# Kernel tuning notes

Measured on AMD Instinct MI355X. Metric: run time of the kernel, lower is better.

Reference implementation:

```python
import jax, jax.numpy as jnp
import numpy as np


def setup_inputs() -> dict:
    key = jax.random.key(0)
    ks = jax.random.split(key, 7)
    G, MC, B = 4, 100, 512
    IN, H, OUT = 456, 400, 10
    return {
        "x": jax.random.normal(ks[0], (B, IN), dtype=jnp.float32),
        "mu1": jax.random.normal(ks[1], (G, IN, H), dtype=jnp.float32),
        "sigma1": jax.random.normal(ks[2], (G, IN, H), dtype=jnp.float32),
        "mu3": jax.random.normal(ks[3], (G, H, OUT), dtype=jnp.float32),
        "sigma3": jax.random.normal(ks[4], (G, H, OUT), dtype=jnp.float32),
        "zeta1": jax.random.normal(ks[5], (G, MC, B, H), dtype=jnp.float32),
        "zeta3": jax.random.normal(ks[6], (G, MC, B, OUT), dtype=jnp.float32),
        "num": 3,
    }


def reference(x, mu1, sigma1, mu3, sigma3, zeta1, zeta3, num):
    # softplus(sigma)^2, the local-reparameterization variance term
    sp2 = lambda s: jnp.square(jnp.log1p(jnp.exp(s)))

    def one_net(m1, s1, m3, s3, z1, z3):
        # layer 1: local reparameterization trick (Kingma et al. 2015)
        g1 = x @ m1                               # [B, H]
        d1 = (x * x) @ sp2(s1)                    # [B, H]
        h = jax.nn.relu(g1 + jnp.sqrt(d1) * z1)   # [MC, B, H] via broadcast
        # layer 2
        g3 = jnp.einsum('mbh,ho->mbo', h, m3)     # [MC, B, OUT]
        d3 = jnp.einsum('mbh,ho->mbo', h * h, sp2(s3))
        o = jax.nn.relu(g3 + jnp.sqrt(d3) * z3)
        p = jax.nn.softmax(o, axis=-1)            # nn.Softmax over class dim
        return p.mean(axis=0)                     # average over MC samples

    G = num + 1
    outs = jax.vmap(one_net)(mu1[:G], sigma1[:G], mu3[:G], sigma3[:G],
                             zeta1[:G], zeta3[:G])  # [G, B, OUT]
    B = x.shape[0]
    # torch.cat((out_0, out_1, ...), dim=1)
    return jnp.transpose(outs, (1, 0, 2)).reshape(B, -1)
```

## Files before the change

### kernel.cpp

```cpp
#include <hip/hip_runtime.h>
#include <math.h>

#define GN  4
#define MCN 100
#define BN  512
#define INN 456
#define HN  400
#define ON  10

__device__ __forceinline__ float sp2f(float s) {
    float l = log1pf(__expf(-fabsf(s)));
    float r = fmaxf(s, 0.0f) + l;
    return r * r;
}

#define DPP_ADD(v, CTRL) \
    ((v) + __int_as_float(__builtin_amdgcn_update_dpp( \
        0, __float_as_int(v), (CTRL), 0xF, 0xF, true)))

__device__ __forceinline__ float reduce16(float v) {
    v = DPP_ADD(v, 0xB1);
    v = DPP_ADD(v, 0x4E);
    v = DPP_ADD(v, 0x124);
    v = DPP_ADD(v, 0x128);
    return v;
}

__global__ __launch_bounds__(256) void k_transpose(
    const float* __restrict__ x, float* __restrict__ xT, float* __restrict__ xxT) {
    __shared__ float tile[64][65];
    int it = blockIdx.x;
    int bt = blockIdx.y;
    int tx = threadIdx.x & 63;
    int ty = threadIdx.x >> 6;
    int i_in = it * 64 + tx;
    #pragma unroll
    for (int r = 0; r < 16; ++r) {
        int row = r * 4 + ty;
        int b = bt * 64 + row;
        tile[row][tx] = (i_in < INN) ? x[b * INN + i_in] : 0.0f;
    }
    __syncthreads();
    #pragma unroll
    for (int r = 0; r < 16; ++r) {
        int row = r * 4 + ty;
        int i = it * 64 + row;
        if (i < INN) {
            float v = tile[tx][row];
            xT[i * BN + bt * 64 + tx]  = v;
            xxT[i * BN + bt * 64 + tx] = v * v;
        }
    }
}

__global__ __launch_bounds__(256) void k_sp(
    const float* __restrict__ sigma1, const float* __restrict__ sigma3,
    float* __restrict__ sp1, float* __restrict__ sp3) {
    int idx = blockIdx.x * 256 + threadIdx.x;
    const int n1 = GN * INN * HN / 4;
    const int n3 = GN * HN * ON / 4;
    if (idx < n1) {
        float4 s = ((const float4*)sigma1)[idx];
        float4 o;
        o.x = sp2f(s.x); o.y = sp2f(s.y); o.z = sp2f(s.z); o.w = sp2f(s.w);
        ((float4*)sp1)[idx] = o;
    } else if (idx < n1 + n3) {
        int k = idx - n1;
        float4 s = ((const float4*)sigma3)[k];
        float4 o;
        o.x = sp2f(s.x); o.y = sp2f(s.y); o.z = sp2f(s.z); o.w = sp2f(s.w);
        ((float4*)sp3)[k] = o;
    }
}

__global__ __launch_bounds__(256) void k_layer1(
    const float* __restrict__ xT, const float* __restrict__ xxT,
    const float* __restrict__ mu1, const float* __restrict__ sp1,
    float* __restrict__ A, float* __restrict__ S) {
    int bt = blockIdx.x;
    int ht = blockIdx.y;
    int g  = blockIdx.z;
    int lane = threadIdx.x & 63;
    int wv   = threadIdx.x >> 6;
    int h = ht * 64 + lane;
    bool hv = h < HN;
    int hc = hv ? h : (HN - 1);
    int b0 = __builtin_amdgcn_readfirstlane(bt * 16 + wv * 4);
    const float* mp = mu1 + (size_t)g * INN * HN + hc;
    const float* pp = sp1 + (size_t)g * INN * HN + hc;
    float accA[4] = {0.f, 0.f, 0.f, 0.f};
    float accD[4] = {0.f, 0.f, 0.f, 0.f};
    #pragma unroll 4
    for (int k = 0; k < INN; ++k) {
        float a = mp[(size_t)k * HN];
        float p = pp[(size_t)k * HN];
        float4 xv  = *(const float4*)(xT  + k * BN + b0);
        float4 xxv = *(const float4*)(xxT + k * BN + b0);
        accA[0] = fmaf(a, xv.x,  accA[0]);
        accA[1] = fmaf(a, xv.y,  accA[1]);
        accA[2] = fmaf(a, xv.z,  accA[2]);
        accA[3] = fmaf(a, xv.w,  accA[3]);
        accD[0] = fmaf(p, xxv.x, accD[0]);
        accD[1] = fmaf(p, xxv.y, accD[1]);
        accD[2] = fmaf(p, xxv.z, accD[2]);
        accD[3] = fmaf(p, xxv.w, accD[3]);
    }
    if (hv) {
        #pragma unroll
        for (int j = 0; j < 4; ++j) {
            size_t o = ((size_t)g * BN + (b0 + j)) * HN + h;
            A[o] = accA[j];
            S[o] = sqrtf(accD[j]);
        }
    }
}

template<int NI>
__device__ __forceinline__ void mc_chunk(
    int g, int b, int mb, int kc, int og, int rgg, int t,
    const float* __restrict__ zeta1, const float* __restrict__ zeta3,
    const float* as_s, const float* wp, float* epi, float* psum) {
    float acc[NI][ON];
    #pragma unroll
    for (int i = 0; i < NI; ++i)
        #pragma unroll
        for (int o = 0; o < ON; ++o) acc[i][o] = 0.0f;

    const float* zp[NI];
    #pragma unroll
    for (int i = 0; i < NI; ++i) {
        int m = mb + rgg + 8 * i;
        int mcl = m < MCN ? m : (MCN - 1);
        zp[i] = zeta1 + ((size_t)(g * MCN + mcl) * BN + b) * HN + kc;
    }

    float zc[NI];
    #pragma unroll
    for (int i = 0; i < NI; ++i) zc[i] = zp[i][0];

    #pragma unroll 1
    for (int j = 0; j < 25; ++j) {
        float zn[NI];
        if (j < 24) {
            #pragma unroll
            for (int i = 0; i < NI; ++i) zn[i] = zp[i][16 * (j + 1)];
        } else {
            #pragma unroll
            for (int i = 0; i < NI; ++i) zn[i] = 0.0f;
        }
        float2 as = *(const float2*)(as_s + 2 * (kc + 16 * j));
        const float* wr = wp + j * 160;
        float2 w01 = *(const float2*)(wr);
        float2 w23 = *(const float2*)(wr + 2);
        float2 w45 = *(const float2*)(wr + 4);
        float2 w67 = *(const float2*)(wr + 6);
        float2 w89 = *(const float2*)(wr + 8);
        #pragma unroll
        for (int i = 0; i < NI; ++i) {
            float hv = fmaxf(0.0f, fmaf(as.y, zc[i], as.x));
            float c = og ? hv * hv : hv;
            acc[i][0] = fmaf(c, w01.x, acc[i][0]);
            acc[i][1] = fmaf(c, w01.y, acc[i][1]);
            acc[i][2] = fmaf(c, w23.x, acc[i][2]);
            acc[i][3] = fmaf(c, w23.y, acc[i][3]);
            acc[i][4] = fmaf(c, w45.x, acc[i][4]);
            acc[i][5] = fmaf(c, w45.y, acc[i][5]);
            acc[i][6] = fmaf(c, w67.x, acc[i][6]);
            acc[i][7] = fmaf(c, w67.y, acc[i][7]);
            acc[i][8] = fmaf(c, w89.x, acc[i][8]);
            acc[i][9] = fmaf(c, w89.y, acc[i][9]);
        }
        #pragma unroll
        for (int i = 0; i < NI; ++i) zc[i] = zn[i];
    }

    #pragma unroll
    for (int i = 0; i < NI; ++i)
        #pragma unroll
        for (int o = 0; o < ON; ++o) acc[i][o] = reduce16(acc[i][o]);

    if (kc == 0) {
        #pragma unroll
        for (int i = 0; i < NI; ++i) {
            int rl = rgg + 8 * i;
            #pragma unroll
            for (int o = 0; o < ON; ++o)
                epi[(rl * ON + o) * 2 + og] = acc[i][o];
        }
    }
    __syncthreads();

    const int NR = NI * 8;
    if (t < NR) {
        int m = mb + t;
        if (m < MCN) {
            const float* z3p = zeta3 + ((size_t)(g * MCN + m) * BN + b) * ON;
            float ov[ON];
            float mx = 0.0f;
            #pragma unroll
            for (int o = 0; o < ON; ++o) {
                float2 gd = *(const float2*)(epi + (t * ON + o) * 2);
                float v = fmaf(sqrtf(gd.y), z3p[o], gd.x);
                v = fmaxf(v, 0.0f);
                ov[o] = v;
                mx = fmaxf(mx, v);
            }
            float se = 0.0f;
            #pragma unroll
            for (int o = 0; o < ON; ++o) { float e = __expf(ov[o] - mx); ov[o] = e; se += e; }
            float r = 1.0f / se;
            #pragma unroll
            for (int o = 0; o < ON; ++o) psum[o] = fmaf(ov[o], r, psum[o]);
        }
    }
    __syncthreads();
}

__global__ __launch_bounds__(256, 4) void k_layer2(
    const float* __restrict__ A, const float* __restrict__ S,
    const float* __restrict__ mu3, const float* __restrict__ sp3,
    const float* __restrict__ zeta1, const float* __restrict__ zeta3,
    float* __restrict__ out) {
    int b = blockIdx.x;
    int g = blockIdx.y;

    __shared__ __align__(16) float w_s[HN * ON];
    __shared__ __align__(16) float v_s[HN * ON];
    __shared__ __align__(16) float as_s[2 * HN];
    __shared__ __align__(16) float epi[32 * ON * 2];
    __shared__ __align__(16) float psh[32 * ON];

    int t = threadIdx.x;

    {
        const float4* wsrc = (const float4*)(mu3 + (size_t)g * HN * ON);
        const float4* vsrc = (const float4*)(sp3 + (size_t)g * HN * ON);
        for (int i = t; i < HN * ON / 4; i += 256) {
            ((float4*)w_s)[i] = wsrc[i];
            ((float4*)v_s)[i] = vsrc[i];
        }
    }
    for (int i = t; i < HN; i += 256) {
        size_t src = ((size_t)g * BN + b) * HN + i;
        as_s[2 * i]     = A[src];
        as_s[2 * i + 1] = S[src];
    }
    __syncthreads();

    int kc  = t & 15;
    int og  = (t >> 4) & 1;
    int rgg = t >> 5;

    const float* wp = (og ? v_s : w_s) + kc * ON;

    float psum[ON];
    #pragma unroll
    for (int o = 0; o < ON; ++o) psum[o] = 0.0f;

    #pragma unroll 1
    for (int c = 0; c < 3; ++c)
        mc_chunk<4>(g, b, c * 32, kc, og, rgg, t, zeta1, zeta3, as_s, wp, epi, psum);
    mc_chunk<1>(g, b, 96, kc, og, rgg, t, zeta1, zeta3, as_s, wp, epi, psum);

    if (t < 32) {
        #pragma unroll
        for (int o = 0; o < ON; ++o) psh[t * ON + o] = psum[o];
    }
    __syncthreads();
    if (t < ON) {
        float s = 0.0f;
        #pragma unroll
        for (int r = 0; r < 32; ++r) s += psh[r * ON + t];
        out[b * (GN * ON) + g * ON + t] = s * (1.0f / MCN);
    }
}

extern "C" void kernel_launch(void* const* d_in, const int* in_sizes, int n_in,
                              void* d_out, int out_size, void* d_ws, size_t ws_size,
                              hipStream_t stream) {
    const float* x      = (const float*)d_in[0];
    const float* mu1    = (const float*)d_in[1];
    const float* sigma1 = (const float*)d_in[2];
    const float* mu3    = (const float*)d_in[3];
    const float* sigma3 = (const float*)d_in[4];
    const float* zeta1  = (const float*)d_in[5];
    const float* zeta3  = (const float*)d_in[6];

    float* ws  = (float*)d_ws;
    float* xT  = ws;
    float* xxT = xT  + INN * BN;
    float* sp1 = xxT + INN * BN;
    float* sp3 = sp1 + GN * INN * HN;
    float* A   = sp3 + GN * HN * ON;
    float* S   = A   + GN * BN * HN;
    float* out = (float*)d_out;

    const int nsp = GN * INN * HN / 4 + GN * HN * ON / 4;
    k_transpose<<<dim3(8, 8), 256, 0, stream>>>(x, xT, xxT);
    k_sp<<<dim3((nsp + 255) / 256), 256, 0, stream>>>(sigma1, sigma3, sp1, sp3);
    k_layer1<<<dim3(32, 7, GN), 256, 0, stream>>>(xT, xxT, mu1, sp1, A, S);
    k_layer2<<<dim3(BN, GN), 256, 0, stream>>>(A, S, mu3, sp3, zeta1, zeta3, out);
}
```

Before: 588.0 us.

## Vectorize zeta1 loads as float4 with transposed layer-2 weights in LDS

Each thread now covers 4 consecutive hidden units per step and loads zeta1 as float4, so the main loop runs 6 iterations plus a scalar tail instead of 25 iterations of scalar loads. The layer-2 weights are stored transposed in shared memory ([OUT][H]) so that each output's 4 consecutive weights come from one float4 LDS read. The goal is fewer, wider global and LDS loads on the bandwidth-bound zeta1 stream. In exchange it uses more registers, so launch bounds drop from 4 to 3 blocks per SIMD, and the weight staging becomes a scalar transposing copy.

Result: faster. 565.9 us (-3.8%).

```diff
diff --git a/kernel.cpp b/kernel.cpp
--- a/kernel.cpp
+++ b/kernel.cpp
@@ -120,6 +120,8 @@
     int g, int b, int mb, int kc, int og, int rgg, int t,
     const float* __restrict__ zeta1, const float* __restrict__ zeta3,
     const float* as_s, const float* wp, float* epi, float* psum) {
+    const int NR = NI * 8;
+
     float acc[NI][ON];
     #pragma unroll
     for (int i = 0; i < NI; ++i)
@@ -131,47 +133,66 @@
     for (int i = 0; i < NI; ++i) {
         int m = mb + rgg + 8 * i;
         int mcl = m < MCN ? m : (MCN - 1);
-        zp[i] = zeta1 + ((size_t)(g * MCN + mcl) * BN + b) * HN + kc;
-    }
-
-    float zc[NI];
-    #pragma unroll
-    for (int i = 0; i < NI; ++i) zc[i] = zp[i][0];
+        zp[i] = zeta1 + ((size_t)(g * MCN + mcl) * BN + b) * HN + 4 * kc;
+    }
+
+    float4 zc[NI];
+    #pragma unroll
+    for (int i = 0; i < NI; ++i) zc[i] = *(const float4*)(zp[i]);
 
     #pragma unroll 1
-    for (int j = 0; j < 25; ++j) {
-        float zn[NI];
-        if (j < 24) {
-            #pragma unroll
-            for (int i = 0; i < NI; ++i) zn[i] = zp[i][16 * (j + 1)];
+    for (int j = 0; j < 6; ++j) {
+        float4 zn[NI];
+        if (j < 5) {
+            #pragma unroll
+            for (int i = 0; i < NI; ++i) zn[i] = *(const float4*)(zp[i] + 64 * (j + 1));
         } else {
             #pragma unroll
-            for (int i = 0; i < NI; ++i) zn[i] = 0.0f;
-        }
-        float2 as = *(const float2*)(as_s + 2 * (kc + 16 * j));
-        const float* wr = wp + j * 160;
-        float2 w01 = *(const float2*)(wr);
-        float2 w23 = *(const float2*)(wr + 2);
-        float2 w45 = *(const float2*)(wr + 4);
-        float2 w67 = *(const float2*)(wr + 6);
-        float2 w89 = *(const float2*)(wr + 8);
+            for (int i = 0; i < NI; ++i) zn[i] = zc[i];
+        }
+        int k0 = 4 * kc + 64 * j;
+        float4 as01 = *(const float4*)(as_s + 2 * k0);
+        float4 as23 = *(const float4*)(as_s + 2 * k0 + 4);
+        float4 W[ON];
+        #pragma unroll
+        for (int o = 0; o < ON; ++o) W[o] = *(const float4*)(wp + o * HN + k0);
         #pragma unroll
         for (int i = 0; i < NI; ++i) {
-            float hv = fmaxf(0.0f, fmaf(as.y, zc[i], as.x));
+            float h0 = fmaxf(0.0f, fmaf(as01.y, zc[i].x, as01.x));
+            float h1 = fmaxf(0.0f, fmaf(as01.w, zc[i].y, as01.z));
+            float h2 = fmaxf(0.0f, fmaf(as23.y, zc[i].z, as23.x));
+            float h3 = fmaxf(0.0f, fmaf(as23.w, zc[i].w, as23.z));
+            float c0 = og ? h0 * h0 : h0;
+            float c1 = og ? h1 * h1 : h1;
+            float c2 = og ? h2 * h2 : h2;
+            float c3 = og ? h3 * h3 : h3;
+            #pragma unroll
+            for (int o = 0; o < ON; ++o) {
+                acc[i][o] = fmaf(c0, W[o].x, acc[i][o]);
+                acc[i][o] = fmaf(c1, W[o].y, acc[i][o]);
+                acc[i][o] = fmaf(c2, W[o].z, acc[i][o]);
+                acc[i][o] = fmaf(c3, W[o].w, acc[i][o]);
+            }
+        }
+        #pragma unroll
+        for (int i = 0; i < NI; ++i) zc[i] = zn[i];
+    }
+
+    {
+        int k = 384 + kc;
+        int toff = 384 - 3 * kc;
+        float2 as = *(const float2*)(as_s + 2 * k);
+        float wt[ON];
+        #pragma unroll
+        for (int o = 0; o < ON; ++o) wt[o] = wp[o * HN + k];
+        #pragma unroll
+        for (int i = 0; i < NI; ++i) {
+            float z = zp[i][toff];
+            float hv = fmaxf(0.0f, fmaf(as.y, z, as.x));
             float c = og ? hv * hv : hv;
-            acc[i][0] = fmaf(c, w01.x, acc[i][0]);
-            acc[i][1] = fmaf(c, w01.y, acc[i][1]);
-            acc[i][2] = fmaf(c, w23.x, acc[i][2]);
-            acc[i][3] = fmaf(c, w23.y, acc[i][3]);
-            acc[i][4] = fmaf(c, w45.x, acc[i][4]);
-            acc[i][5] = fmaf(c, w45.y, acc[i][5]);
-            acc[i][6] = fmaf(c, w67.x, acc[i][6]);
-            acc[i][7] = fmaf(c, w67.y, acc[i][7]);
-            acc[i][8] = fmaf(c, w89.x, acc[i][8]);
-            acc[i][9] = fmaf(c, w89.y, acc[i][9]);
-        }
-        #pragma unroll
-        for (int i = 0; i < NI; ++i) zc[i] = zn[i];
+            #pragma unroll
+            for (int o = 0; o < ON; ++o) acc[i][o] = fmaf(c, wt[o], acc[i][o]);
+        }
     }
 
     #pragma unroll
@@ -190,7 +211,6 @@
     }
     __syncthreads();
 
-    const int NR = NI * 8;
     if (t < NR) {
         int m = mb + t;
         if (m < MCN) {
@@ -216,7 +236,7 @@
     __syncthreads();
 }
 
-__global__ __launch_bounds__(256, 4) void k_layer2(
+__global__ __launch_bounds__(256, 3) void k_layer2(
     const float* __restrict__ A, const float* __restrict__ S,
     const float* __restrict__ mu3, const float* __restrict__ sp3,
     const float* __restrict__ zeta1, const float* __restrict__ zeta3,
@@ -224,8 +244,8 @@
     int b = blockIdx.x;
     int g = blockIdx.y;
 
-    __shared__ __align__(16) float w_s[HN * ON];
-    __shared__ __align__(16) float v_s[HN * ON];
+    __shared__ __align__(16) float wT_s[ON * HN];
+    __shared__ __align__(16) float vT_s[ON * HN];
     __shared__ __align__(16) float as_s[2 * HN];
     __shared__ __align__(16) float epi[32 * ON * 2];
     __shared__ __align__(16) float psh[32 * ON];
@@ -233,11 +253,12 @@
     int t = threadIdx.x;
 
     {
-        const float4* wsrc = (const float4*)(mu3 + (size_t)g * HN * ON);
-        const float4* vsrc = (const float4*)(sp3 + (size_t)g * HN * ON);
-        for (int i = t; i < HN * ON / 4; i += 256) {
-            ((float4*)w_s)[i] = wsrc[i];
-            ((float4*)v_s)[i] = vsrc[i];
+        const float* wsrc = mu3 + (size_t)g * HN * ON;
+        const float* vsrc = sp3 + (size_t)g * HN * ON;
+        for (int i = t; i < HN * ON; i += 256) {
+            int h = i / ON, o = i - h * ON;
+            wT_s[o * HN + h] = wsrc[i];
+            vT_s[o * HN + h] = vsrc[i];
         }
     }
     for (int i = t; i < HN; i += 256) {
@@ -251,7 +272,7 @@
     int og  = (t >> 4) & 1;
     int rgg = t >> 5;
 
-    const float* wp = (og ? v_s : w_s) + kc * ON;
+    const float* wp = og ? vT_s : wT_s;
 
     float psum[ON];
     #pragma unroll
```
